# Performance work log

Hardware: AMD Instinct MI355X
Metric: run time of the kernel (lower is better)

The kernel has to match this reference:

```python
import jax, jax.numpy as jnp
import numpy as np

B, T, H, NB, D, DH = 2, 8192, 16, 32, 1024, 128


def setup_inputs() -> dict:
    key = jax.random.key(0)
    ks = jax.random.split(key, 4)
    theta_path = jax.random.normal(ks[0], (B, T, H, NB), dtype=jnp.float32)
    content_emb = jax.random.normal(ks[1], (B, T, D), dtype=jnp.float32)
    W1 = jax.random.normal(ks[2], (D, DH), dtype=jnp.float32) / np.sqrt(D)
    b1 = jnp.zeros((DH,), dtype=jnp.float32)
    W2 = jax.random.normal(ks[3], (DH, H * NB), dtype=jnp.float32) / np.sqrt(DH)
    b2 = jnp.zeros((H * NB,), dtype=jnp.float32)
    log_Q = jnp.full((H, NB), -3.0, dtype=jnp.float32)  # torch init: full(-3.0)
    log_R = jnp.full((H, NB), 1.0, dtype=jnp.float32)   # torch init: full(1.0)
    return {"theta_path": theta_path, "content_emb": content_emb,
            "W1": W1, "b1": b1, "W2": W2, "b2": b2,
            "log_Q": log_Q, "log_R": log_R}


def _steady_state_K(log_Q, log_R):
    # closed-form scalar DARE: K* = (P+Q)/(P+Q+R), P = (-Q + sqrt(Q^2+4QR))/2
    Q = jnp.exp(log_Q)
    R = jnp.exp(log_R)
    P_post = 0.5 * (-Q + jnp.sqrt(Q * Q + 4.0 * Q * R))
    P_pred = P_post + Q
    return P_pred / (P_pred + R)


def _parallel_affine_scan(nu, K_star):
    # d_t = K * sum_{s<=t} (1-K)^(t-s) nu_s via zero-padded FFT convolution
    b, t, h, nb = nu.shape
    alpha = 1.0 - K_star                                   # (H, NB)
    k_idx = jnp.arange(t, dtype=nu.dtype)
    kernel = K_star[..., None] * (alpha[..., None] ** k_idx)  # (H, NB, T)
    pad_len = 2 * t
    kernel_fft = jnp.fft.rfft(kernel, n=pad_len, axis=-1)     # (H, NB, pad/2+1)
    nu_perm = jnp.transpose(nu, (0, 2, 3, 1))                 # (B, H, NB, T)
    nu_fft = jnp.fft.rfft(nu_perm, n=pad_len, axis=-1)
    conv = jnp.fft.irfft(nu_fft * kernel_fft[None], n=pad_len, axis=-1)[..., :t]
    return jnp.transpose(conv, (0, 3, 1, 2))                  # (B, T, H, NB)


def reference(theta_path, content_emb, W1, b1, W2, b2, log_Q, log_R):
    b, t, h, nb = theta_path.shape
    hid = jax.nn.gelu(content_emb @ W1 + b1, approximate=False)  # exact GELU (torch default)
    z_raw = (hid @ W2 + b2).reshape(b, t, h, nb)
    z = jnp.pi * jnp.tanh(z_raw)
    diff = z - theta_path
    nu = jnp.arctan2(jnp.sin(diff), jnp.cos(diff))  # wrap to (-pi, pi]
    K_star = _steady_state_K(log_Q, log_R)
    d = _parallel_affine_scan(nu, K_star)
    theta_hat = theta_path + d
    return theta_hat, d, K_star
```

## Files before the change

kernel.cpp:

```cpp
#include <hip/hip_runtime.h>
#include <math.h>

#define Bq 2
#define Tq 8192
#define Dq 1024
#define DHq 128
#define HNq 512
#define Mq (Bq*Tq)
#define NELEM ((size_t)Mq*HNq)
#define CHL 16
#define NCHK (Mq/CHL)
#define CH8 8
#define NC8 (Mq/CH8)
#define CPS8 (Tq/CH8)

typedef _Float16 half8 __attribute__((ext_vector_type(8)));
typedef float    f32x4 __attribute__((ext_vector_type(4)));

#define SC_LO  2048.0f
#define ISC_LO 4.8828125e-4f


__device__ __forceinline__ float gelu_exact(float x) {
    return 0.5f * x * (1.0f + erff(x * 0.7071067811865475f));
}

__device__ __forceinline__ float wrap_pi(float d) {
    return fmaf(-6.283185307179586f, rintf(d * 0.15915494309189535f), d);
}

__device__ __forceinline__ void gl16(const void* g, void* ldsDst) {
    __builtin_amdgcn_global_load_lds(
        (const __attribute__((address_space(1))) unsigned int*)g,
        (__attribute__((address_space(3))) unsigned int*)ldsDst, 16, 0, 0);
}

__global__ __launch_bounds__(64) void p0_pack(
    const float* __restrict__ W1, const float* __restrict__ W2,
    const float* __restrict__ lq, const float* __restrict__ lr,
    _Float16* __restrict__ w1h, _Float16* __restrict__ w1l,
    _Float16* __restrict__ w2h, _Float16* __restrict__ w2l,
    float* __restrict__ Karr, float* __restrict__ Aarr,
    float* __restrict__ kout)
{
    const int l = threadIdx.x;
    const int u = blockIdx.x;
    if (u == 384) {
        #pragma unroll
        for (int i = 0; i < 8; ++i) {
            int col = i * 64 + l;
            float Q = expf(lq[col]);
            float R = expf(lr[col]);
            float P = 0.5f * (-Q + sqrtf(fmaf(Q, Q, 4.0f * Q * R)));
            float Pp = P + Q;
            float K = Pp / (Pp + R);
            Karr[col] = K;
            Aarr[col] = 1.0f - K;
            kout[col] = K;
        }
        return;
    }
    const float* W; _Float16 *ph, *pl; int ncols, kt, ct, unit;
    if (u < 256) { unit = u;       kt = unit >> 3; ct = unit & 7;  W = W1; ph = w1h; pl = w1l; ncols = 128; }
    else         { unit = u - 256; kt = unit >> 5; ct = unit & 31; W = W2; ph = w2h; pl = w2l; ncols = 512; }
    const int col = ct * 16 + (l & 15);
    const int k0  = kt * 32 + ((l >> 4) * 8);
    half8 hv, lv;
    #pragma unroll
    for (int j = 0; j < 8; ++j) {
        float x = W[(size_t)(k0 + j) * ncols + col];
        _Float16 h = (_Float16)x;
        hv[j] = h;
        lv[j] = (_Float16)((x - (float)h) * SC_LO);
    }
    size_t off = ((size_t)unit * 64 + l) * 8;
    *(half8*)(ph + off) = hv;
    *(half8*)(pl + off) = lv;
}

__global__ __launch_bounds__(512, 1) void k1_mfma(
    const float* __restrict__ A, const _Float16* __restrict__ w1h,
    const _Float16* __restrict__ w1l, const float* __restrict__ b1,
    _Float16* __restrict__ hidH, _Float16* __restrict__ hidL)
{
    __shared__ char lds[49152];
    const int tid = threadIdx.x;
    const int w = tid >> 6, l = tid & 63;
    const int lrow = l & 15, lq = l >> 4;
    const int rq = w >> 1, ns = w & 1;
    const int rowb = blockIdx.x * 64;

    const int arow = tid >> 3;
    const int ac4  = (tid & 7) ^ (arow & 7);
    const float* aSrc = A + (size_t)(rowb + arow) * Dq + ac4 * 4;
    const _Float16* bplane = (w & 1) ? w1l : w1h;
    const _Float16* bSrc0 = bplane + ((size_t)(w >> 1) * 64 + l) * 8;
    const _Float16* bSrc1 = bplane + ((size_t)(4 + (w >> 1)) * 64 + l) * 8;

#define STAGE(slot, s) do {                                                   \
        gl16(aSrc + (s) * 32, lds + (slot) * 8192 + w * 1024);                \
        gl16(bSrc0 + (size_t)(s) * 4096,                                     \
             lds + 16384 + (slot) * 16384 + w * 1024);                        \
        gl16(bSrc1 + (size_t)(s) * 4096,                                     \
             lds + 16384 + (slot) * 16384 + 8192 + w * 1024);                 \
    } while (0)

    const int aRdRow = (rq * 16 + lrow) * 128;
    const int aRd0 = ((lq * 2 + 0) ^ (lrow & 7)) * 16;
    const int aRd1 = ((lq * 2 + 1) ^ (lrow & 7)) * 16;
    const int ns4 = ns * 4;

    STAGE(0, 0);
    STAGE(1, 1);

    f32x4 accM[2][4] = {};
    f32x4 accC[2][4] = {};

#define ITER(s, KH) do {                                                      \
        asm volatile("s_waitcnt vmcnt(3)" ::: "memory");                      \
        __builtin_amdgcn_sched_barrier(0);                                    \
        __builtin_amdgcn_s_barrier();                                         \
        __builtin_amdgcn_sched_barrier(0);                                    \
        char* As_ = lds + ((s) & 1) * 8192;                                   \
        char* Bs_ = lds + 16384 + ((s) & 1) * 16384;                          \
        f32x4 a0_ = *(const f32x4*)(As_ + aRdRow + aRd0);                     \
        f32x4 a1_ = *(const f32x4*)(As_ + aRdRow + aRd1);                     \
        half8 bh_[4], bl_[4];                                                 \
        _Pragma("unroll")                                                     \
        for (int ct_ = 0; ct_ < 4; ++ct_) {                                   \
            bh_[ct_] = *(const half8*)(Bs_ + ((ns4 + ct_) * 2 + 0) * 1024 + l * 16); \
            bl_[ct_] = *(const half8*)(Bs_ + ((ns4 + ct_) * 2 + 1) * 1024 + l * 16); \
        }                                                                     \
        asm volatile("s_waitcnt lgkmcnt(0)" ::: "memory");                    \
        __builtin_amdgcn_sched_barrier(0);                                    \
        __builtin_amdgcn_s_barrier();                                         \
        __builtin_amdgcn_sched_barrier(0);                                    \
        { int sp_ = (s) + 2; if (sp_ > 31) sp_ = 31; STAGE((s) & 1, sp_); }   \
        half8 ah_, alo_;                                                      \
        { float xs_[8] = {a0_[0], a0_[1], a0_[2], a0_[3],                     \
                          a1_[0], a1_[1], a1_[2], a1_[3]};                    \
          _Pragma("unroll")                                                   \
          for (int j_ = 0; j_ < 8; ++j_) {                                    \
              _Float16 h_ = (_Float16)xs_[j_];                                \
              ah_[j_]  = h_;                                                  \
              alo_[j_] = (_Float16)((xs_[j_] - (float)h_) * SC_LO);           \
          } }                                                                 \
        _Pragma("unroll")                                                     \
        for (int ct_ = 0; ct_ < 4; ++ct_) {                                   \
            accM[KH][ct_] = __builtin_amdgcn_mfma_f32_16x16x32_f16(ah_,  bh_[ct_], accM[KH][ct_], 0, 0, 0); \
            accC[KH][ct_] = __builtin_amdgcn_mfma_f32_16x16x32_f16(ah_,  bl_[ct_], accC[KH][ct_], 0, 0, 0); \
            accC[KH][ct_] = __builtin_amdgcn_mfma_f32_16x16x32_f16(alo_, bh_[ct_], accC[KH][ct_], 0, 0, 0); \
        }                                                                     \
    } while (0)

    #pragma unroll 2
    for (int s = 0; s < 16; ++s)  ITER(s, 0);
    #pragma unroll 2
    for (int s = 16; s < 32; ++s) ITER(s, 1);

#undef ITER
#undef STAGE

    asm volatile("s_waitcnt vmcnt(0)" ::: "memory");
    __syncthreads();
    float* ldsR = (float*)lds;
    #pragma unroll
    for (int ct = 0; ct < 4; ++ct) {
        const int ctG = ns4 + ct;
        #pragma unroll
        for (int r = 0; r < 4; ++r)
            ldsR[(rq * 16 + lq * 4 + r) * 132 + ctG * 16 + lrow] =
                fmaf(accC[0][ct][r], ISC_LO, accM[0][ct][r]) +
                fmaf(accC[1][ct][r], ISC_LO, accM[1][ct][r]);
    }
    __syncthreads();

    #pragma unroll
    for (int uh = 0; uh < 2; ++uh) {
        const int u  = w * 2 + uh;
        const int cl = u >> 2;
        const int kt = u & 3;
        const int dh0 = kt * 32 + lq * 8;
        const float* rp = ldsR + (cl * 16 + lrow) * 132 + dh0;
        f32x4 s0 = *(const f32x4*)rp;
        f32x4 s1 = *(const f32x4*)(rp + 4);
        f32x4 bb0 = *(const f32x4*)(b1 + dh0);
        f32x4 bb1 = *(const f32x4*)(b1 + dh0 + 4);
        half8 hv, lv;
        #pragma unroll
        for (int j = 0; j < 4; ++j) {
            float g = gelu_exact(s0[j] + bb0[j]);
            _Float16 h = (_Float16)g;
            hv[j] = h; lv[j] = (_Float16)((g - (float)h) * SC_LO);
        }
        #pragma unroll
        for (int j = 0; j < 4; ++j) {
            float g = gelu_exact(s1[j] + bb1[j]);
            _Float16 h = (_Float16)g;
            hv[4 + j] = h; lv[4 + j] = (_Float16)((g - (float)h) * SC_LO);
        }
        size_t off = (((size_t)(blockIdx.x * 4 + cl) * 4 + kt) * 64 + l) * 8;
        *(half8*)(hidH + off) = hv;
        *(half8*)(hidL + off) = lv;
    }
}

__global__ __launch_bounds__(256, 4) void k2a_mfma(
    const _Float16* __restrict__ hidH, const _Float16* __restrict__ hidL,
    const _Float16* __restrict__ w2h, const _Float16* __restrict__ w2l,
    const float* __restrict__ b2, const float* __restrict__ theta,
    const float* __restrict__ Karr, const float* __restrict__ Aarr,
    float* __restrict__ nuG, float* __restrict__ carries8)
{
    __shared__ float nuL[16][516];
    const int tid = threadIdx.x;
    const int w = tid >> 6, l = tid & 63;
    const int lrow = l & 15, lq = l >> 4;
    const int blk = blockIdx.x;

    f32x4 accM[8] = {};
    f32x4 accC[8] = {};
    #pragma unroll
    for (int kt = 0; kt < 4; ++kt) {
        size_t aoff = (((size_t)blk * 4 + kt) * 64 + l) * 8;
        const half8 ah  = *(const half8*)(hidH + aoff);
        const half8 alo = *(const half8*)(hidL + aoff);
        #pragma unroll
        for (int ct = 0; ct < 8; ++ct) {
            const int ctG = w * 8 + ct;
            size_t boff = (((size_t)kt * 32 + ctG) * 64 + l) * 8;
            const half8 bh = *(const half8*)(w2h + boff);
            const half8 bl = *(const half8*)(w2l + boff);
            accM[ct] = __builtin_amdgcn_mfma_f32_16x16x32_f16(ah,  bh, accM[ct], 0, 0, 0);
            accC[ct] = __builtin_amdgcn_mfma_f32_16x16x32_f16(ah,  bl, accC[ct], 0, 0, 0);
            accC[ct] = __builtin_amdgcn_mfma_f32_16x16x32_f16(alo, bh, accC[ct], 0, 0, 0);
        }
    }

    const float PI_F = 3.14159265358979323846f;
    #pragma unroll
    for (int ct = 0; ct < 8; ++ct) {
        const int col = w * 128 + ct * 16 + lrow;
        const float bb = b2[col];
        #pragma unroll
        for (int r = 0; r < 4; ++r) {
            const int row = blk * 16 + lq * 4 + r;
            float z = fmaf(accC[ct][r], ISC_LO, accM[ct][r]) + bb;
            float t = PI_F * tanhf(z);
            size_t io = (size_t)row * HNq + col;
            accM[ct][r] = wrap_pi(t - theta[io]);
        }
    }
    #pragma unroll
    for (int ct = 0; ct < 8; ++ct)
        #pragma unroll
        for (int r = 0; r < 4; ++r)
            nuL[lq * 4 + r][w * 128 + ct * 16 + lrow] = accM[ct][r];
    __syncthreads();

    #pragma unroll
    for (int cc = 0; cc < 2; ++cc) {
        const int col = tid + cc * 256;
        const float K = Karr[col], al = Aarr[col];
        #pragma unroll
        for (int sub = 0; sub < 2; ++sub) {
            float c = 0.0f;
            #pragma unroll
            for (int r = 0; r < 8; ++r)
                c = fmaf(al, c, K * nuL[sub * 8 + r][col]);
            carries8[(size_t)(blk * 2 + sub) * HNq + col] = c;
        }
    }
    f32x4* dst = (f32x4*)nuG + (size_t)blk * 2048;
    #pragma unroll
    for (int it = 0; it < 8; ++it) {
        const int g = tid + it * 256;
        const int row = g >> 7, cw = g & 127;
        dst[g] = *(const f32x4*)&nuL[row][cw * 4];
    }
}

__global__ __launch_bounds__(256) void k2b_scan(
    const float* __restrict__ theta, const float* __restrict__ Karr,
    const float* __restrict__ Aarr, const float* __restrict__ carries8,
    float* __restrict__ nud, float* __restrict__ theta_hat)
{
    const int tid = threadIdx.x;
    const int sub = tid >> 7, cg = tid & 127, c0 = cg * 4;
    const int chunk = blockIdx.x * 2 + sub;
    const int cloc = chunk & (CPS8 - 1);
    const int seq0 = chunk - cloc;

    const f32x4 K4 = *(const f32x4*)(Karr + c0);
    const f32x4 A4 = *(const f32x4*)(Aarr + c0);
    f32x4 A8;
    #pragma unroll
    for (int j = 0; j < 4; ++j) {
        float a2 = A4[j] * A4[j];
        float a4 = a2 * a2;
        A8[j] = a4 * a4;
    }
    float amax = fmaxf(fmaxf(A8[0], A8[1]), fmaxf(A8[2], A8[3]));
    int n = cloc;
    if (amax <= 0.0f) {
        n = 0;
    } else {
        float ln = logf(amax);
        if (ln < -1e-9f) {
            int nn = (int)ceilf(-34.0f / ln);
            if (nn < n) n = nn;
        }
    }
    f32x4 s = {0.0f, 0.0f, 0.0f, 0.0f};
    for (int j = cloc - n; j < cloc; ++j) {
        f32x4 cv = *(const f32x4*)(carries8 + (size_t)(seq0 + j) * HNq + c0);
        s = A8 * s + cv;
    }

    const size_t base = (size_t)chunk * CH8 * HNq + c0;
    #pragma unroll
    for (int r = 0; r < CH8; ++r) {
        const size_t idx = base + (size_t)r * HNq;
        f32x4 nu = *(const f32x4*)(nud + idx);
        f32x4 th = *(const f32x4*)(theta + idx);
        s = A4 * s + K4 * nu;
        *(f32x4*)(nud + idx) = s;
        *(f32x4*)(theta_hat + idx) = th + s;
    }
}

extern "C" void kernel_launch(void* const* d_in, const int* in_sizes, int n_in,
                              void* d_out, int out_size, void* d_ws, size_t ws_size,
                              hipStream_t stream) {
    const float* theta   = (const float*)d_in[0];
    const float* content = (const float*)d_in[1];
    const float* W1      = (const float*)d_in[2];
    const float* b1      = (const float*)d_in[3];
    const float* W2      = (const float*)d_in[4];
    const float* b2      = (const float*)d_in[5];
    const float* logQ    = (const float*)d_in[6];
    const float* logR    = (const float*)d_in[7];

    float* out       = (float*)d_out;
    float* theta_hat = out;
    float* dbuf      = out + NELEM;
    float* kout      = out + 2 * NELEM;

    _Float16* w1h  = (_Float16*)d_ws;
    _Float16* w1l  = w1h + 131072;
    _Float16* w2h  = w1l + 131072;
    _Float16* w2l  = w2h + 65536;
    _Float16* hidH = w2l + 65536;
    _Float16* hidL = hidH + 2097152;
    float* Karr    = (float*)(hidL + 2097152);
    float* Aarr    = Karr + 512;
    float* carries8 = Aarr + 512;

    p0_pack<<<dim3(385), 64, 0, stream>>>(W1, W2, logQ, logR,
                                          w1h, w1l, w2h, w2l, Karr, Aarr, kout);
    k1_mfma<<<dim3(Mq / 64), 512, 0, stream>>>(content, w1h, w1l, b1, hidH, hidL);
    k2a_mfma<<<dim3(NCHK), 256, 0, stream>>>(hidH, hidL, w2h, w2l, b2, theta,
                                             Karr, Aarr, dbuf, carries8);
    k2b_scan<<<dim3(NC8 / 2), 256, 0, stream>>>(theta, Karr, Aarr, carries8,
                                                dbuf, theta_hat);
}
```

Measured before the change: 209.6 us.

## Make k2a persistent over four row chunks with register-resident W2 and LDS double buffer

```diff
diff --git a/kernel.cpp b/kernel.cpp
--- a/kernel.cpp
+++ b/kernel.cpp
@@ -205,79 +205,116 @@
     }
 }
 
-__global__ __launch_bounds__(256, 4) void k2a_mfma(
+__global__ __launch_bounds__(512, 2) void k2a_mfma(
     const _Float16* __restrict__ hidH, const _Float16* __restrict__ hidL,
     const _Float16* __restrict__ w2h, const _Float16* __restrict__ w2l,
     const float* __restrict__ b2, const float* __restrict__ theta,
     const float* __restrict__ Karr, const float* __restrict__ Aarr,
     float* __restrict__ nuG, float* __restrict__ carries8)
 {
-    __shared__ float nuL[16][516];
+    __shared__ __align__(16) char lds[49408];
+    float* nuL = (float*)(lds + 16384);
     const int tid = threadIdx.x;
     const int w = tid >> 6, l = tid & 63;
     const int lrow = l & 15, lq = l >> 4;
     const int blk = blockIdx.x;
 
-    f32x4 accM[8] = {};
-    f32x4 accC[8] = {};
-    #pragma unroll
-    for (int kt = 0; kt < 4; ++kt) {
-        size_t aoff = (((size_t)blk * 4 + kt) * 64 + l) * 8;
-        const half8 ah  = *(const half8*)(hidH + aoff);
-        const half8 alo = *(const half8*)(hidL + aoff);
-        #pragma unroll
-        for (int ct = 0; ct < 8; ++ct) {
-            const int ctG = w * 8 + ct;
-            size_t boff = (((size_t)kt * 32 + ctG) * 64 + l) * 8;
-            const half8 bh = *(const half8*)(w2h + boff);
-            const half8 bl = *(const half8*)(w2l + boff);
-            accM[ct] = __builtin_amdgcn_mfma_f32_16x16x32_f16(ah,  bh, accM[ct], 0, 0, 0);
-            accC[ct] = __builtin_amdgcn_mfma_f32_16x16x32_f16(ah,  bl, accC[ct], 0, 0, 0);
-            accC[ct] = __builtin_amdgcn_mfma_f32_16x16x32_f16(alo, bh, accC[ct], 0, 0, 0);
-        }
-    }
+    const _Float16* aplane = (w & 1) ? hidL : hidH;
+    const _Float16* aSrc = aplane + ((size_t)(blk * 4) * 4 + (w >> 1)) * 512
+                                  + (size_t)l * 8;
+#define STAGEA(slot, c) gl16(aSrc + (size_t)(c) * 2048, lds + (slot) * 8192 + w * 1024)
+
+    STAGEA(0, 0);
+    STAGEA(1, 1);
+
+    half8 Bh[4][4], Bl[4][4];
+    #pragma unroll
+    for (int kt = 0; kt < 4; ++kt)
+        #pragma unroll
+        for (int i = 0; i < 4; ++i) {
+            size_t boff = (((size_t)kt * 32 + (w * 4 + i)) * 64 + l) * 8;
+            Bh[kt][i] = *(const half8*)(w2h + boff);
+            Bl[kt][i] = *(const half8*)(w2l + boff);
+        }
+
+    const float Kv = Karr[tid], Av = Aarr[tid];
+    float b2v[4];
+    #pragma unroll
+    for (int i = 0; i < 4; ++i) b2v[i] = b2[w * 64 + i * 16 + lrow];
 
     const float PI_F = 3.14159265358979323846f;
-    #pragma unroll
-    for (int ct = 0; ct < 8; ++ct) {
-        const int col = w * 128 + ct * 16 + lrow;
-        const float bb = b2[col];
-        #pragma unroll
-        for (int r = 0; r < 4; ++r) {
-            const int row = blk * 16 + lq * 4 + r;
-            float z = fmaf(accC[ct][r], ISC_LO, accM[ct][r]) + bb;
-            float t = PI_F * tanhf(z);
-            size_t io = (size_t)row * HNq + col;
-            accM[ct][r] = wrap_pi(t - theta[io]);
-        }
-    }
-    #pragma unroll
-    for (int ct = 0; ct < 8; ++ct)
-        #pragma unroll
-        for (int r = 0; r < 4; ++r)
-            nuL[lq * 4 + r][w * 128 + ct * 16 + lrow] = accM[ct][r];
-    __syncthreads();
-
-    #pragma unroll
-    for (int cc = 0; cc < 2; ++cc) {
-        const int col = tid + cc * 256;
-        const float K = Karr[col], al = Aarr[col];
+
+    #pragma unroll
+    for (int c = 0; c < 4; ++c) {
+        asm volatile("s_waitcnt vmcnt(1)" ::: "memory");
+        __builtin_amdgcn_sched_barrier(0);
+        __builtin_amdgcn_s_barrier();
+        __builtin_amdgcn_sched_barrier(0);
+        char* sb = lds + (c & 1) * 8192;
+        half8 ah[4], al[4];
+        #pragma unroll
+        for (int kt = 0; kt < 4; ++kt) {
+            ah[kt] = *(const half8*)(sb + (kt * 2 + 0) * 1024 + l * 16);
+            al[kt] = *(const half8*)(sb + (kt * 2 + 1) * 1024 + l * 16);
+        }
+        asm volatile("s_waitcnt lgkmcnt(0)" ::: "memory");
+        __builtin_amdgcn_sched_barrier(0);
+        __builtin_amdgcn_s_barrier();
+        __builtin_amdgcn_sched_barrier(0);
+        { int cp = c + 2; if (cp > 3) cp = 3; STAGEA(c & 1, cp); }
+
+        f32x4 accM[4] = {};
+        f32x4 accC[4] = {};
+        #pragma unroll
+        for (int kt = 0; kt < 4; ++kt)
+            #pragma unroll
+            for (int i = 0; i < 4; ++i) {
+                accM[i] = __builtin_amdgcn_mfma_f32_16x16x32_f16(ah[kt], Bh[kt][i], accM[i], 0, 0, 0);
+                accC[i] = __builtin_amdgcn_mfma_f32_16x16x32_f16(ah[kt], Bl[kt][i], accC[i], 0, 0, 0);
+                accC[i] = __builtin_amdgcn_mfma_f32_16x16x32_f16(al[kt], Bh[kt][i], accC[i], 0, 0, 0);
+            }
+
+        const int row0 = (blk * 4 + c) * 16 + lq * 4;
+        float th[4][4];
+        #pragma unroll
+        for (int i = 0; i < 4; ++i) {
+            const int col = w * 64 + i * 16 + lrow;
+            #pragma unroll
+            for (int r = 0; r < 4; ++r)
+                th[i][r] = theta[(size_t)(row0 + r) * HNq + col];
+        }
+        #pragma unroll
+        for (int i = 0; i < 4; ++i) {
+            const int col = w * 64 + i * 16 + lrow;
+            #pragma unroll
+            for (int r = 0; r < 4; ++r) {
+                float z = fmaf(accC[i][r], ISC_LO, accM[i][r]) + b2v[i];
+                float t = PI_F * tanhf(z);
+                nuL[(lq * 4 + r) * 516 + col] = wrap_pi(t - th[i][r]);
+            }
+        }
+        asm volatile("s_waitcnt lgkmcnt(0)" ::: "memory");
+        __builtin_amdgcn_sched_barrier(0);
+        __builtin_amdgcn_s_barrier();
+        __builtin_amdgcn_sched_barrier(0);
+
         #pragma unroll
         for (int sub = 0; sub < 2; ++sub) {
-            float c = 0.0f;
+            float cacc = 0.0f;
             #pragma unroll
             for (int r = 0; r < 8; ++r)
-                c = fmaf(al, c, K * nuL[sub * 8 + r][col]);
-            carries8[(size_t)(blk * 2 + sub) * HNq + col] = c;
-        }
-    }
-    f32x4* dst = (f32x4*)nuG + (size_t)blk * 2048;
-    #pragma unroll
-    for (int it = 0; it < 8; ++it) {
-        const int g = tid + it * 256;
-        const int row = g >> 7, cw = g & 127;
-        dst[g] = *(const f32x4*)&nuL[row][cw * 4];
-    }
+                cacc = fmaf(Av, cacc, Kv * nuL[(sub * 8 + r) * 516 + tid]);
+            carries8[(size_t)((blk * 4 + c) * 2 + sub) * HNq + tid] = cacc;
+        }
+        f32x4* dst = (f32x4*)nuG + (size_t)(blk * 4 + c) * 2048;
+        #pragma unroll
+        for (int it = 0; it < 4; ++it) {
+            const int g = tid + it * 512;
+            const int row = g >> 7, cw = g & 127;
+            dst[g] = *(const f32x4*)&nuL[row * 516 + cw * 4];
+        }
+    }
+#undef STAGEA
 }
 
 __global__ __launch_bounds__(256) void k2b_scan(
@@ -359,8 +396,8 @@
     p0_pack<<<dim3(385), 64, 0, stream>>>(W1, W2, logQ, logR,
                                           w1h, w1l, w2h, w2l, Karr, Aarr, kout);
     k1_mfma<<<dim3(Mq / 64), 512, 0, stream>>>(content, w1h, w1l, b1, hidH, hidL);
-    k2a_mfma<<<dim3(NCHK), 256, 0, stream>>>(hidH, hidL, w2h, w2l, b2, theta,
-                                             Karr, Aarr, dbuf, carries8);
+    k2a_mfma<<<dim3(NCHK / 4), 512, 0, stream>>>(hidH, hidL, w2h, w2l, b2, theta,
+                                                 Karr, Aarr, dbuf, carries8);
     k2b_scan<<<dim3(NC8 / 2), 256, 0, stream>>>(theta, Karr, Aarr, carries8,
                                                 dbuf, theta_hat);
 }
```

New measurement: 214.2 us. 2.2% more time.
